# Kernel tuning notes

Measured on AMD Instinct MI355X. Metric: run time of the kernel, lower is better.

Reference implementation:

```python
import jax, jax.numpy as jnp
import numpy as np

EMBED = 1024
HEADS = 16
DK = EMBED // HEADS


def setup_inputs() -> dict:
    key = jax.random.key(0)
    ks = jax.random.split(key, 6)
    B, S = 2, 2048
    scale = 1.0 / np.sqrt(EMBED)
    x = jax.random.normal(ks[0], (B, S, EMBED), dtype=jnp.float32)
    Wq = jax.random.normal(ks[1], (EMBED, EMBED), dtype=jnp.float32) * scale
    Wk = jax.random.normal(ks[2], (EMBED, EMBED), dtype=jnp.float32) * scale
    Wv = jax.random.normal(ks[3], (EMBED, EMBED), dtype=jnp.float32) * scale
    Wo = jax.random.normal(ks[4], (EMBED, EMBED), dtype=jnp.float32) * scale
    qw = jnp.zeros((HEADS, 1), dtype=jnp.float32)  # quantum_weight, init quantum_scale=0
    return {"x": x, "Wq": Wq, "Wk": Wk, "Wv": Wv, "Wo": Wo, "qw": qw}


def reference(x, Wq, Wk, Wv, Wo, qw):
    B, S, E = x.shape
    # nn.Linear with no bias: y = x @ W.T; split heads -> [B,H,S,Dk]
    def proj(W):
        return (x @ W.T).reshape(B, S, HEADS, DK).transpose(0, 2, 1, 3)
    q, k, v = proj(Wq), proj(Wk), proj(Wv)
    scores = jnp.einsum('bhsd,bhtd->bhst', q, k) / np.sqrt(DK)
    attn = jax.nn.softmax(scores, axis=-1)  # dropout in eval mode: identity
    classical = jnp.einsum('bhst,bhtd->bhsd', attn, v)
    w = jax.nn.sigmoid(qw)[:, :, None]  # [H,1,1] per-head mixing weight
    out = w * jnp.sin(classical) + (1.0 - w) * classical
    out = out.transpose(0, 2, 1, 3).reshape(B, S, E)
    return out @ Wo.T
```

## Files before the change

kernel.cpp:

```cpp
#include <hip/hip_runtime.h>
#include <math.h>

constexpr int Ec  = 1024;
constexpr int Hc  = 16;
constexpr int DKc = 64;
constexpr int Bc  = 2;
constexpr int Sc  = 2048;
constexpr int Mc  = Bc * Sc;

typedef _Float16 half8 __attribute__((ext_vector_type(8)));
typedef _Float16 half4 __attribute__((ext_vector_type(4)));
typedef float    floatx4 __attribute__((ext_vector_type(4)));

#define MFMA16(a, b, c) __builtin_amdgcn_mfma_f32_16x16x32_f16(a, b, c, 0, 0, 0)

__device__ __forceinline__ void async_lds16(const _Float16* g, _Float16* l)
{
    __builtin_amdgcn_global_load_lds(
        (const __attribute__((address_space(1))) unsigned int*)g,
        (__attribute__((address_space(3))) unsigned int*)l, 16, 0, 0);
}

__global__ __launch_bounds__(256)
void convert_to_h(const float4* __restrict__ x,
                  const float4* __restrict__ wq,
                  const float4* __restrict__ wk,
                  const float4* __restrict__ wv,
                  const float4* __restrict__ wo,
                  half4* __restrict__ dst)
{
    const int i = blockIdx.x * 256 + threadIdx.x;
    const float4* src; int off;
    if      (i < 1048576) { src = x;  off = i; }
    else if (i < 1310720) { src = wq; off = i - 1048576; }
    else if (i < 1572864) { src = wk; off = i - 1310720; }
    else if (i < 1835008) { src = wv; off = i - 1572864; }
    else                  { src = wo; off = i - 1835008; }
    const float4 v = src[off];
    half4 o;
    o.x = (_Float16)v.x; o.y = (_Float16)v.y;
    o.z = (_Float16)v.z; o.w = (_Float16)v.w;
    dst[i] = o;
}

__device__ __forceinline__ void mfma_gemm_core64(const _Float16* __restrict__ A,
                                                 const _Float16* __restrict__ Bw,
                                                 int m0, int n0,
                                                 _Float16* As, _Float16* Bs,
                                                 floatx4 acc[4][4])
{
    const int tid  = threadIdx.x;
    const int wave = tid >> 6, lane = tid & 63;
    const int l16  = lane & 15, quad = lane >> 4;
    const int wrow = (wave >> 1) * 64, wcol = (wave & 1) * 64;

    const int srow8  = lane >> 3;
    const int schunk = (lane & 7) ^ (srow8 & 7);
    const _Float16* ga = A  + (size_t)(m0 + wave * 32 + srow8) * Ec + schunk * 8;
    const _Float16* gb = Bw + (size_t)(n0 + wave * 32 + srow8) * Ec + schunk * 8;
    _Float16* lA = As + (size_t)(wave * 32) * 64;
    _Float16* lB = Bs + (size_t)(wave * 32) * 64;

    for (int kt = 0; kt < Ec; kt += 64) {
#pragma unroll
        for (int c = 0; c < 4; ++c) {
            async_lds16(ga + (size_t)(c * 8) * Ec + kt, lA + c * 512);
            async_lds16(gb + (size_t)(c * 8) * Ec + kt, lB + c * 512);
        }
        __syncthreads();

        half8 af[4][2], bf[4][2];
#pragma unroll
        for (int i = 0; i < 4; ++i) {
            const int ra = wrow + i * 16 + l16;
            const int rb = wcol + i * 16 + l16;
#pragma unroll
            for (int kc = 0; kc < 2; ++kc) {
                af[i][kc] = *(const half8*)&As[ra * 64 + (((quad + kc * 4) ^ (ra & 7)) * 8)];
                bf[i][kc] = *(const half8*)&Bs[rb * 64 + (((quad + kc * 4) ^ (rb & 7)) * 8)];
            }
        }
#pragma unroll
        for (int i = 0; i < 4; ++i)
#pragma unroll
            for (int j = 0; j < 4; ++j) {
                acc[i][j] = MFMA16(af[i][0], bf[j][0], acc[i][j]);
                acc[i][j] = MFMA16(af[i][1], bf[j][1], acc[i][j]);
            }
        __syncthreads();
    }
}

__global__ __launch_bounds__(256)
void gemm_qkv_mfma(const _Float16* __restrict__ xh,
                   const _Float16* __restrict__ wqh,
                   const _Float16* __restrict__ wkh,
                   const _Float16* __restrict__ wvh,
                   _Float16* __restrict__ Qh,
                   _Float16* __restrict__ Kh,
                   _Float16* __restrict__ VTh)
{
    __shared__ __align__(16) _Float16 As[128 * 64];
    __shared__ __align__(16) _Float16 Bs[128 * 64];
    const int z = blockIdx.z;
    const _Float16* W = (z == 0) ? wqh : (z == 1) ? wkh : wvh;
    const int m0 = blockIdx.y * 128, n0 = blockIdx.x * 128;

    floatx4 acc[4][4] = {};
    mfma_gemm_core64(xh, W, m0, n0, As, Bs, acc);

    const int tid  = threadIdx.x;
    const int wave = tid >> 6, lane = tid & 63;
    const int l16  = lane & 15, quad = lane >> 4;
    const int wrow = (wave >> 1) * 64, wcol = (wave & 1) * 64;

    if (z == 2) {
#pragma unroll
        for (int i = 0; i < 4; ++i)
#pragma unroll
            for (int j = 0; j < 4; ++j) {
                const int n  = n0 + wcol + j * 16 + l16;
                const int hh = n >> 6, d = n & 63;
                const int mb = m0 + wrow + i * 16 + quad * 4;
                const int bb = mb >> 11, s = mb & (Sc - 1);
                half4 pk;
#pragma unroll
                for (int r = 0; r < 4; ++r) pk[r] = (_Float16)acc[i][j][r];
                *(half4*)&VTh[((size_t)((bb * Hc + hh) * DKc + d)) * Sc + s] = pk;
            }
    } else {
        _Float16* out = (z == 0) ? Qh : Kh;
        const float scale = (z == 0) ? 0.125f : 1.0f;
#pragma unroll
        for (int i = 0; i < 4; ++i)
#pragma unroll
            for (int j = 0; j < 4; ++j) {
                const int n = n0 + wcol + j * 16 + l16;
#pragma unroll
                for (int r = 0; r < 4; ++r) {
                    const int m = m0 + wrow + i * 16 + quad * 4 + r;
                    out[(size_t)m * Ec + n] = (_Float16)(acc[i][j][r] * scale);
                }
            }
    }
}

__global__ __launch_bounds__(256)
void gemm_out_mfma(const _Float16* __restrict__ A,
                   const _Float16* __restrict__ W,
                   float* __restrict__ C)
{
    __shared__ __align__(16) _Float16 As[128 * 64];
    __shared__ __align__(16) _Float16 Bs[64 * 64];
    const int m0 = blockIdx.y * 128, n0 = blockIdx.x * 64;

    const int tid  = threadIdx.x;
    const int wave = tid >> 6, lane = tid & 63;
    const int l16  = lane & 15, quad = lane >> 4;
    const int wrow = (wave >> 1) * 64, wcol = (wave & 1) * 32;

    const int srow8  = lane >> 3;
    const int schunk = (lane & 7) ^ (srow8 & 7);
    const _Float16* ga = A + (size_t)(m0 + wave * 32 + srow8) * Ec + schunk * 8;
    const _Float16* gb = W + (size_t)(n0 + wave * 16 + srow8) * Ec + schunk * 8;
    _Float16* lA = As + (size_t)(wave * 32) * 64;
    _Float16* lB = Bs + (size_t)(wave * 16) * 64;

    floatx4 acc[4][2] = {};

    for (int kt = 0; kt < Ec; kt += 64) {
#pragma unroll
        for (int c = 0; c < 4; ++c)
            async_lds16(ga + (size_t)(c * 8) * Ec + kt, lA + c * 512);
#pragma unroll
        for (int c = 0; c < 2; ++c)
            async_lds16(gb + (size_t)(c * 8) * Ec + kt, lB + c * 512);
        __syncthreads();

        half8 af[4][2], bf[2][2];
#pragma unroll
        for (int i = 0; i < 4; ++i) {
            const int ra = wrow + i * 16 + l16;
#pragma unroll
            for (int kc = 0; kc < 2; ++kc)
                af[i][kc] = *(const half8*)&As[ra * 64 + (((quad + kc * 4) ^ (ra & 7)) * 8)];
        }
#pragma unroll
        for (int j = 0; j < 2; ++j) {
            const int rb = wcol + j * 16 + l16;
#pragma unroll
            for (int kc = 0; kc < 2; ++kc)
                bf[j][kc] = *(const half8*)&Bs[rb * 64 + (((quad + kc * 4) ^ (rb & 7)) * 8)];
        }
#pragma unroll
        for (int i = 0; i < 4; ++i)
#pragma unroll
            for (int j = 0; j < 2; ++j) {
                acc[i][j] = MFMA16(af[i][0], bf[j][0], acc[i][j]);
                acc[i][j] = MFMA16(af[i][1], bf[j][1], acc[i][j]);
            }
        __syncthreads();
    }

#pragma unroll
    for (int i = 0; i < 4; ++i)
#pragma unroll
        for (int j = 0; j < 2; ++j) {
            const int n = n0 + wcol + j * 16 + l16;
#pragma unroll
            for (int r = 0; r < 4; ++r) {
                const int m = m0 + wrow + i * 16 + quad * 4 + r;
                C[(size_t)m * Ec + n] = acc[i][j][r];
            }
        }
}

__global__ __launch_bounds__(256)
void flash_attn(const _Float16* __restrict__ Qh,
                const _Float16* __restrict__ Kh,
                const _Float16* __restrict__ VTh,
                const float* __restrict__ qw,
                _Float16* __restrict__ Mixh)
{
    constexpr int BM = 128, BN = 64, LDH = 72;
    __shared__ _Float16 Kt[BN][LDH];
    __shared__ _Float16 Vt[DKc][LDH];
    __shared__ _Float16 Ps[BM][LDH];

    const int tid  = threadIdx.x;
    const int wave = tid >> 6, lane = tid & 63;
    const int quad = lane >> 4, l16 = lane & 15;
    const int q0 = blockIdx.x * BM;
    const int bh = blockIdx.y;
    const int h  = bh & (Hc - 1), b = bh >> 4;

    half8 aq[2][2];
#pragma unroll
    for (int u = 0; u < 2; ++u) {
        const _Float16* qp = Qh + (size_t)(b * Sc + q0 + wave * 32 + u * 16 + l16) * Ec
                                + h * DKc + quad * 8;
        aq[u][0] = *(const half8*)qp;
        aq[u][1] = *(const half8*)(qp + 32);
    }

    const int srow = tid >> 2;
    const int sseg = (tid & 3) * 16;
    const _Float16* Kg = Kh + (size_t)(b * Sc + srow) * Ec + h * DKc + sseg;
    const _Float16* Vg = VTh + ((size_t)(bh * DKc + srow)) * Sc + sseg;

    half8 kr0 = *(const half8*)Kg, kr1 = *(const half8*)(Kg + 8);
    half8 vr0 = *(const half8*)Vg, vr1 = *(const half8*)(Vg + 8);
    Kg += (size_t)BN * Ec; Vg += BN;
    *(half8*)&Kt[srow][sseg]     = kr0;
    *(half8*)&Kt[srow][sseg + 8] = kr1;

    floatx4 o[2][4] = {};
    float l_run[2] = {0.f, 0.f};

    for (int n = 0; n < Sc / BN; ++n) {
        __syncthreads();
        *(half8*)&Vt[srow][sseg]     = vr0;
        *(half8*)&Vt[srow][sseg + 8] = vr1;
        const bool more = (n + 1 < Sc / BN);
        if (more) {
            kr0 = *(const half8*)Kg; kr1 = *(const half8*)(Kg + 8);
            vr0 = *(const half8*)Vg; vr1 = *(const half8*)(Vg + 8);
            Kg += (size_t)BN * Ec; Vg += BN;
        }

        floatx4 st[2][4];
#pragma unroll
        for (int i = 0; i < 4; ++i) {
            const half8 ak0 = *(const half8*)&Kt[i * 16 + l16][quad * 8];
            const half8 ak1 = *(const half8*)&Kt[i * 16 + l16][32 + quad * 8];
            const floatx4 z = {0.f, 0.f, 0.f, 0.f};
            st[0][i] = MFMA16(ak1, aq[0][1], MFMA16(ak0, aq[0][0], z));
            st[1][i] = MFMA16(ak1, aq[1][1], MFMA16(ak0, aq[1][0], z));
        }

#pragma unroll
        for (int u = 0; u < 2; ++u) {
            const int prow = wave * 32 + u * 16 + l16;
#pragma unroll
            for (int i = 0; i < 4; ++i) {
                const float p0 = __expf(st[u][i][0]);
                const float p1 = __expf(st[u][i][1]);
                const float p2 = __expf(st[u][i][2]);
                const float p3 = __expf(st[u][i][3]);
                l_run[u] += (p0 + p1) + (p2 + p3);
                half4 pk;
                pk.x = (_Float16)p0; pk.y = (_Float16)p1;
                pk.z = (_Float16)p2; pk.w = (_Float16)p3;
                *(half4*)&Ps[prow][i * 16 + quad * 4] = pk;
            }
        }
        __syncthreads();

        half8 ap[2][2];
#pragma unroll
        for (int u = 0; u < 2; ++u) {
            const _Float16* pp = &Ps[wave * 32 + u * 16 + l16][quad * 8];
            ap[u][0] = *(const half8*)pp;
            ap[u][1] = *(const half8*)(pp + 32);
        }
#pragma unroll
        for (int jd = 0; jd < 4; ++jd) {
            const half8 bv0 = *(const half8*)&Vt[jd * 16 + l16][quad * 8];
            const half8 bv1 = *(const half8*)&Vt[jd * 16 + l16][32 + quad * 8];
#pragma unroll
            for (int u = 0; u < 2; ++u) {
                o[u][jd] = MFMA16(ap[u][0], bv0, o[u][jd]);
                o[u][jd] = MFMA16(ap[u][1], bv1, o[u][jd]);
            }
        }

        if (more) {
            *(half8*)&Kt[srow][sseg]     = kr0;
            *(half8*)&Kt[srow][sseg + 8] = kr1;
        }
    }

    const float wmix = 1.f / (1.f + __expf(-qw[h]));
#pragma unroll
    for (int u = 0; u < 2; ++u) {
        l_run[u] += __shfl_xor(l_run[u], 16);
        l_run[u] += __shfl_xor(l_run[u], 32);
    }
#pragma unroll
    for (int u = 0; u < 2; ++u)
#pragma unroll
        for (int r = 0; r < 4; ++r) {
            const float l = __shfl(l_run[u], (lane & 48) | (quad * 4 + r));
            const float inv = 1.f / l;
            const int m = q0 + wave * 32 + u * 16 + quad * 4 + r;
            _Float16* mp = Mixh + (size_t)(b * Sc + m) * Ec + h * DKc;
#pragma unroll
            for (int jd = 0; jd < 4; ++jd) {
                const float v = o[u][jd][r] * inv;
                mp[jd * 16 + l16] = (_Float16)(wmix * __sinf(v) + (1.f - wmix) * v);
            }
        }
}

extern "C" void kernel_launch(void* const* d_in, const int* in_sizes, int n_in,
                              void* d_out, int out_size, void* d_ws, size_t ws_size,
                              hipStream_t stream)
{
    const float* x  = (const float*)d_in[0];
    const float* Wq = (const float*)d_in[1];
    const float* Wk = (const float*)d_in[2];
    const float* Wv = (const float*)d_in[3];
    const float* Wo = (const float*)d_in[4];
    const float* qw = (const float*)d_in[5];
    float* out = (float*)d_out;

    _Float16* hb   = (_Float16*)d_ws;
    _Float16* xh   = hb;
    _Float16* wqh  = hb + (size_t)4 * 1024 * 1024;
    _Float16* wkh  = hb + (size_t)5 * 1024 * 1024;
    _Float16* wvh  = hb + (size_t)6 * 1024 * 1024;
    _Float16* woh  = hb + (size_t)7 * 1024 * 1024;
    _Float16* Qh   = hb + (size_t)8 * 1024 * 1024;
    _Float16* Kh   = hb + (size_t)12 * 1024 * 1024;
    _Float16* VTh  = hb + (size_t)16 * 1024 * 1024;
    _Float16* mixh = hb + (size_t)20 * 1024 * 1024;

    convert_to_h<<<dim3(8192), dim3(256), 0, stream>>>(
        (const float4*)x, (const float4*)Wq, (const float4*)Wk,
        (const float4*)Wv, (const float4*)Wo, (half4*)hb);

    gemm_qkv_mfma<<<dim3(Ec / 128, Mc / 128, 3), dim3(256), 0, stream>>>(
        xh, wqh, wkh, wvh, Qh, Kh, VTh);

    flash_attn<<<dim3(Sc / 128, Bc * Hc), dim3(256), 0, stream>>>(
        Qh, Kh, VTh, qw, mixh);

    gemm_out_mfma<<<dim3(Ec / 64, Mc / 128), dim3(256), 0, stream>>>(
        mixh, woh, out);
}
```

Before: 191.8 us.

## Split attention over the key dimension into two halves with a reduction kernel

The flash attention grid gains a z-dimension of 2, so each block processes half of the key/value sequence. Each block writes unnormalized fp16 partial outputs and float row sums. A new reduce_mix kernel adds the two partials, normalizes them, and applies the sigmoid-weighted sin mix. This doubles the number of attention blocks to improve occupancy and latency hiding, at the cost of an extra launch and extra global traffic for the partials. Keeping unnormalized sums in fp16 adds some precision and overflow risk.

```diff
diff --git a/kernel.cpp b/kernel.cpp
--- a/kernel.cpp
+++ b/kernel.cpp
@@ -219,10 +219,12 @@
 void flash_attn(const _Float16* __restrict__ Qh,
                 const _Float16* __restrict__ Kh,
                 const _Float16* __restrict__ VTh,
-                const float* __restrict__ qw,
-                _Float16* __restrict__ Mixh)
+                _Float16* __restrict__ Op0,
+                _Float16* __restrict__ Op1,
+                float* __restrict__ lp)
 {
     constexpr int BM = 128, BN = 64, LDH = 72;
+    constexpr int NIT = (Sc / 2) / BN;
     __shared__ _Float16 Kt[BN][LDH];
     __shared__ _Float16 Vt[DKc][LDH];
     __shared__ _Float16 Ps[BM][LDH];
@@ -232,7 +234,9 @@
     const int quad = lane >> 4, l16 = lane & 15;
     const int q0 = blockIdx.x * BM;
     const int bh = blockIdx.y;
+    const int kz = blockIdx.z;
     const int h  = bh & (Hc - 1), b = bh >> 4;
+    const int k0 = kz * (Sc / 2);
 
     half8 aq[2][2];
 #pragma unroll
@@ -245,8 +249,8 @@
 
     const int srow = tid >> 2;
     const int sseg = (tid & 3) * 16;
-    const _Float16* Kg = Kh + (size_t)(b * Sc + srow) * Ec + h * DKc + sseg;
-    const _Float16* Vg = VTh + ((size_t)(bh * DKc + srow)) * Sc + sseg;
+    const _Float16* Kg = Kh + (size_t)(b * Sc + k0 + srow) * Ec + h * DKc + sseg;
+    const _Float16* Vg = VTh + ((size_t)(bh * DKc + srow)) * Sc + k0 + sseg;
 
     half8 kr0 = *(const half8*)Kg, kr1 = *(const half8*)(Kg + 8);
     half8 vr0 = *(const half8*)Vg, vr1 = *(const half8*)(Vg + 8);
@@ -257,11 +261,11 @@
     floatx4 o[2][4] = {};
     float l_run[2] = {0.f, 0.f};
 
-    for (int n = 0; n < Sc / BN; ++n) {
+    for (int n = 0; n < NIT; ++n) {
         __syncthreads();
         *(half8*)&Vt[srow][sseg]     = vr0;
         *(half8*)&Vt[srow][sseg + 8] = vr1;
-        const bool more = (n + 1 < Sc / BN);
+        const bool more = (n + 1 < NIT);
         if (more) {
             kr0 = *(const half8*)Kg; kr1 = *(const half8*)(Kg + 8);
             vr0 = *(const half8*)Vg; vr1 = *(const half8*)(Vg + 8);
@@ -320,26 +324,53 @@
         }
     }
 
-    const float wmix = 1.f / (1.f + __expf(-qw[h]));
+    _Float16* Ob = kz ? Op1 : Op0;
 #pragma unroll
     for (int u = 0; u < 2; ++u) {
         l_run[u] += __shfl_xor(l_run[u], 16);
         l_run[u] += __shfl_xor(l_run[u], 32);
-    }
-#pragma unroll
-    for (int u = 0; u < 2; ++u)
+        if (quad == 0)
+            lp[(size_t)kz * (Bc * Hc * Sc) + (size_t)bh * Sc
+               + q0 + wave * 32 + u * 16 + l16] = l_run[u];
 #pragma unroll
         for (int r = 0; r < 4; ++r) {
-            const float l = __shfl(l_run[u], (lane & 48) | (quad * 4 + r));
-            const float inv = 1.f / l;
             const int m = q0 + wave * 32 + u * 16 + quad * 4 + r;
-            _Float16* mp = Mixh + (size_t)(b * Sc + m) * Ec + h * DKc;
-#pragma unroll
-            for (int jd = 0; jd < 4; ++jd) {
-                const float v = o[u][jd][r] * inv;
-                mp[jd * 16 + l16] = (_Float16)(wmix * __sinf(v) + (1.f - wmix) * v);
-            }
-        }
+            _Float16* mp = Ob + (size_t)(b * Sc + m) * Ec + h * DKc;
+#pragma unroll
+            for (int jd = 0; jd < 4; ++jd)
+                mp[jd * 16 + l16] = (_Float16)o[u][jd][r];
+        }
+    }
+}
+
+__global__ __launch_bounds__(256)
+void reduce_mix(const half4* __restrict__ Op0,
+                const half4* __restrict__ Op1,
+                const float* __restrict__ lp,
+                const float* __restrict__ qw,
+                half4* __restrict__ Mixh)
+{
+    const int i = blockIdx.x * 256 + threadIdx.x;
+    const int row = i >> 8;
+    const int h   = (i & 255) >> 4;
+    const int b   = row >> 11;
+    const int s   = row & (Sc - 1);
+    const int bh  = b * Hc + h;
+
+    const float l0 = lp[(size_t)bh * Sc + s];
+    const float l1 = lp[(size_t)(Bc * Hc * Sc) + (size_t)bh * Sc + s];
+    const float inv = 1.f / (l0 + l1);
+    const float wmix = 1.f / (1.f + __expf(-qw[h]));
+
+    const half4 a = Op0[i];
+    const half4 c = Op1[i];
+    half4 o;
+#pragma unroll
+    for (int t = 0; t < 4; ++t) {
+        const float v = ((float)a[t] + (float)c[t]) * inv;
+        o[t] = (_Float16)(wmix * __sinf(v) + (1.f - wmix) * v);
+    }
+    Mixh[i] = o;
 }
 
 extern "C" void kernel_launch(void* const* d_in, const int* in_sizes, int n_in,
@@ -354,16 +385,20 @@
     const float* qw = (const float*)d_in[5];
     float* out = (float*)d_out;
 
+    constexpr size_t M1 = 1024 * 1024;
     _Float16* hb   = (_Float16*)d_ws;
     _Float16* xh   = hb;
-    _Float16* wqh  = hb + (size_t)4 * 1024 * 1024;
-    _Float16* wkh  = hb + (size_t)5 * 1024 * 1024;
-    _Float16* wvh  = hb + (size_t)6 * 1024 * 1024;
-    _Float16* woh  = hb + (size_t)7 * 1024 * 1024;
-    _Float16* Qh   = hb + (size_t)8 * 1024 * 1024;
-    _Float16* Kh   = hb + (size_t)12 * 1024 * 1024;
-    _Float16* VTh  = hb + (size_t)16 * 1024 * 1024;
-    _Float16* mixh = hb + (size_t)20 * 1024 * 1024;
+    _Float16* wqh  = hb + 4 * M1;
+    _Float16* wkh  = hb + 5 * M1;
+    _Float16* wvh  = hb + 6 * M1;
+    _Float16* woh  = hb + 7 * M1;
+    _Float16* Qh   = hb + 8 * M1;
+    _Float16* Kh   = hb + 12 * M1;
+    _Float16* VTh  = hb + 16 * M1;
+    _Float16* mixh = hb + 20 * M1;
+    _Float16* Op0  = hb;
+    _Float16* Op1  = hb + 24 * M1;
+    float*    lp   = (float*)(hb + 28 * M1);
 
     convert_to_h<<<dim3(8192), dim3(256), 0, stream>>>(
         (const float4*)x, (const float4*)Wq, (const float4*)Wk,
@@ -372,8 +407,11 @@
     gemm_qkv_mfma<<<dim3(Ec / 128, Mc / 128, 3), dim3(256), 0, stream>>>(
         xh, wqh, wkh, wvh, Qh, Kh, VTh);
 
-    flash_attn<<<dim3(Sc / 128, Bc * Hc), dim3(256), 0, stream>>>(
-        Qh, Kh, VTh, qw, mixh);
+    flash_attn<<<dim3(Sc / 128, Bc * Hc, 2), dim3(256), 0, stream>>>(
+        Qh, Kh, VTh, Op0, Op1, lp);
+
+    reduce_mix<<<dim3(4096), dim3(256), 0, stream>>>(
+        (const half4*)Op0, (const half4*)Op1, lp, qw, (half4*)mixh);
 
     gemm_out_mfma<<<dim3(Ec / 64, Mc / 128), dim3(256), 0, stream>>>(
         mixh, woh, out);
```

Result: slower. 199.3 us (+3.9%).
